# Performance work log

Hardware: AMD Instinct MI355X
Metric: run time of the kernel (lower is better)

Reference implementation:

```python
import jax, jax.numpy as jnp
import numpy as np

B, S, D = 32, 2048, 1024
E, K = 64, 8
N_TAGS = 128


def setup_inputs() -> dict:
    key = jax.random.key(0)
    k1, k2, k3, k4, k5, k6 = jax.random.split(key, 6)
    hidden_states = jax.random.normal(k1, (B, S, D), dtype=jnp.float32)
    subw_indices = jax.random.randint(k2, (B, E, K), 0, S, dtype=jnp.int32)
    subw_counts = jax.random.randint(k3, (B, E), 1, K + 1, dtype=jnp.int32)
    num_entities = jax.random.randint(k4, (B,), 1, E + 1, dtype=jnp.int32)
    fc_w = jax.random.normal(k5, (N_TAGS, D), dtype=jnp.float32) * (1.0 / np.sqrt(D))
    fc_b = jax.random.normal(k6, (N_TAGS,), dtype=jnp.float32) * 0.01
    return {
        "hidden_states": hidden_states,
        "subw_indices": subw_indices,
        "subw_counts": subw_counts,
        "num_entities": num_entities,
        "fc_w": fc_w,
        "fc_b": fc_b,
    }


def reference(hidden_states, subw_indices, subw_counts, num_entities, fc_w, fc_b):
    # Gather subword embeddings: [B, E, K, D]
    flat_idx = subw_indices.reshape(B, E * K)                      # [B, E*K]
    gathered = jnp.take_along_axis(
        hidden_states, flat_idx[:, :, None], axis=1
    ).reshape(B, E, K, D)
    # Mask padded subword slots and mean-pool per entity
    subw_mask = (jnp.arange(K)[None, None, :] < subw_counts[:, :, None])  # [B,E,K]
    subw_mask = subw_mask.astype(hidden_states.dtype)
    ent_emb = jnp.einsum("bekd,bek->bed", gathered, subw_mask)
    ent_emb = ent_emb / subw_counts[:, :, None].astype(hidden_states.dtype)
    # Zero-pad entities past num_entities (original pads with zero_emb)
    ent_mask = (jnp.arange(E)[None, :] < num_entities[:, None])    # [B,E]
    ent_emb = ent_emb * ent_mask[:, :, None].astype(hidden_states.dtype)
    # fc applied to all positions (padded rows yield the bias, as in original)
    logits = jnp.einsum("bed,td->bet", ent_emb, fc_w) + fc_b
    return logits
```

## Files before the change

### kernel.cpp

```cpp
#include <hip/hip_runtime.h>

#define BB 32
#define SS 2048
#define DD 1024
#define EE 64
#define KK 8
#define TT 128
#define MM (BB * EE)

#define KSPLIT 8
#define KCHUNK (DD / KSPLIT)
#define MT 32

typedef __attribute__((ext_vector_type(8))) short short8;
typedef __attribute__((ext_vector_type(4))) float f32x4;

__device__ __forceinline__ unsigned short f2bf(float f) {
    union { float f; unsigned int u; } v; v.f = f;
    unsigned int u = v.u + 0x7FFFu + ((v.u >> 16) & 1u);
    return (unsigned short)(u >> 16);
}

__global__ __launch_bounds__(256) void pool_kernel(
    const float* __restrict__ hs,
    const int*   __restrict__ subw_idx,
    const int*   __restrict__ subw_cnt,
    const int*   __restrict__ num_ent,
    const float* __restrict__ fc_w,
    unsigned short* __restrict__ entb,
    unsigned short* __restrict__ wb)
{
    const int be = blockIdx.x;
    const int b  = be >> 6;
    const int e  = be & 63;
    const int t  = threadIdx.x;

    const int cnt = subw_cnt[be];
    const int ne  = num_ent[b];
    const float scale = (e < ne) ? (1.0f / (float)cnt) : 0.0f;

    const int* idxp = subw_idx + (size_t)be * KK;

    float4 acc = make_float4(0.f, 0.f, 0.f, 0.f);
    #pragma unroll
    for (int k = 0; k < KK; ++k) {
        if (k < cnt) {
            const int s = idxp[k];
            const float4* row = (const float4*)(hs + ((size_t)b * SS + s) * DD);
            float4 v = row[t];
            acc.x += v.x; acc.y += v.y; acc.z += v.z; acc.w += v.w;
        }
    }
    ushort4 o;
    o.x = f2bf(acc.x * scale); o.y = f2bf(acc.y * scale);
    o.z = f2bf(acc.z * scale); o.w = f2bf(acc.w * scale);
    *(ushort4*)(entb + (size_t)be * DD + 4 * t) = o;

    if (t < 64) {
        const int j = be * 64 + t;
        wb[j] = f2bf(fc_w[j]);
    }
}

__global__ __launch_bounds__(256) void fc_mfma_kernel(
    const unsigned short* __restrict__ entb,
    const unsigned short* __restrict__ wb,
    float* __restrict__ part)
{
    __shared__ unsigned short As[MT][32];
    __shared__ unsigned short Bs[TT][32];

    const int bx = blockIdx.x;
    const int mt = bx >> 3;
    const int ks = bx & (KSPLIT - 1);
    const int t  = threadIdx.x;
    const int wid  = t >> 6;
    const int lane = t & 63;

    const int msub  = (wid & 1) * 16;
    const int nbase = (wid >> 1) * 64;

    const int k0 = ks * KCHUNK;

    f32x4 acc0 = {0.f,0.f,0.f,0.f}, acc1 = {0.f,0.f,0.f,0.f};
    f32x4 acc2 = {0.f,0.f,0.f,0.f}, acc3 = {0.f,0.f,0.f,0.f};

    const int lm = lane & 15;
    const int lq = (lane >> 4) * 8;

    for (int kc = 0; kc < KCHUNK; kc += 32) {
        if (t < 128) {
            const int m = t >> 2, s = t & 3;
            *(float4*)&As[m][s * 8] =
                *(const float4*)(entb + (size_t)(mt * MT + m) * DD + k0 + kc + s * 8);
        }
        #pragma unroll
        for (int j = 0; j < 2; ++j) {
            const int i = t + j * 256;
            const int n = i >> 2, s = i & 3;
            *(float4*)&Bs[n][s * 8] =
                *(const float4*)(wb + (size_t)n * DD + k0 + kc + s * 8);
        }
        __syncthreads();

        short8 a = *(const short8*)&As[msub + lm][lq];
        short8 b0 = *(const short8*)&Bs[nbase +  0 + lm][lq];
        short8 b1 = *(const short8*)&Bs[nbase + 16 + lm][lq];
        short8 b2 = *(const short8*)&Bs[nbase + 32 + lm][lq];
        short8 b3 = *(const short8*)&Bs[nbase + 48 + lm][lq];

        acc0 = __builtin_amdgcn_mfma_f32_16x16x32_bf16(a, b0, acc0, 0, 0, 0);
        acc1 = __builtin_amdgcn_mfma_f32_16x16x32_bf16(a, b1, acc1, 0, 0, 0);
        acc2 = __builtin_amdgcn_mfma_f32_16x16x32_bf16(a, b2, acc2, 0, 0, 0);
        acc3 = __builtin_amdgcn_mfma_f32_16x16x32_bf16(a, b3, acc3, 0, 0, 0);
        __syncthreads();
    }

    float* outp = part + (size_t)ks * MM * TT;
    const int mrow = mt * MT + msub + (lane >> 4) * 4;
    const int ncol = nbase + (lane & 15);
    #pragma unroll
    for (int r = 0; r < 4; ++r) {
        const size_t base = (size_t)(mrow + r) * TT + ncol;
        outp[base +  0] = acc0[r];
        outp[base + 16] = acc1[r];
        outp[base + 32] = acc2[r];
        outp[base + 48] = acc3[r];
    }
}

__global__ __launch_bounds__(256) void reduce_kernel(
    const float* __restrict__ part,
    const float* __restrict__ fc_b,
    float* __restrict__ out)
{
    const int i = blockIdx.x * 256 + threadIdx.x;
    float4 s = *(const float4*)(fc_b + (i & 31) * 4);
    #pragma unroll
    for (int k = 0; k < KSPLIT; ++k) {
        float4 p = *(const float4*)(part + (size_t)k * MM * TT + 4 * i);
        s.x += p.x; s.y += p.y; s.z += p.z; s.w += p.w;
    }
    *(float4*)(out + 4 * (size_t)i) = s;
}

extern "C" void kernel_launch(void* const* d_in, const int* in_sizes, int n_in,
                              void* d_out, int out_size, void* d_ws, size_t ws_size,
                              hipStream_t stream) {
    const float* hs       = (const float*)d_in[0];
    const int*   subw_idx = (const int*)  d_in[1];
    const int*   subw_cnt = (const int*)  d_in[2];
    const int*   num_ent  = (const int*)  d_in[3];
    const float* fc_w     = (const float*)d_in[4];
    const float* fc_b     = (const float*)d_in[5];
    float*       out      = (float*)d_out;

    unsigned short* entb = (unsigned short*)d_ws;
    unsigned short* wb   = (unsigned short*)((char*)d_ws + (size_t)MM * DD * 2);
    float*          part = (float*)((char*)d_ws + (size_t)MM * DD * 2 + (size_t)TT * DD * 2);

    pool_kernel<<<MM, 256, 0, stream>>>(hs, subw_idx, subw_cnt, num_ent,
                                        fc_w, entb, wb);
    fc_mfma_kernel<<<(MM / MT) * KSPLIT, 256, 0, stream>>>(entb, wb, part);
    reduce_kernel<<<(MM * TT / 4) / 256, 256, 0, stream>>>(part, fc_b, out);
}
```

Before: 318.4 us.

## Fuse entity pooling and weight conversion into the MFMA fc kernel

```diff
diff --git a/kernel.cpp b/kernel.cpp
--- a/kernel.cpp
+++ b/kernel.cpp
@@ -11,6 +11,7 @@
 #define KSPLIT 8
 #define KCHUNK (DD / KSPLIT)
 #define MT 32
+#define LSTR 136
 
 typedef __attribute__((ext_vector_type(8))) short short8;
 typedef __attribute__((ext_vector_type(4))) float f32x4;
@@ -21,54 +22,16 @@
     return (unsigned short)(u >> 16);
 }
 
-__global__ __launch_bounds__(256) void pool_kernel(
+__global__ __launch_bounds__(256) void fc_fused_kernel(
     const float* __restrict__ hs,
     const int*   __restrict__ subw_idx,
     const int*   __restrict__ subw_cnt,
     const int*   __restrict__ num_ent,
     const float* __restrict__ fc_w,
-    unsigned short* __restrict__ entb,
-    unsigned short* __restrict__ wb)
-{
-    const int be = blockIdx.x;
-    const int b  = be >> 6;
-    const int e  = be & 63;
-    const int t  = threadIdx.x;
-
-    const int cnt = subw_cnt[be];
-    const int ne  = num_ent[b];
-    const float scale = (e < ne) ? (1.0f / (float)cnt) : 0.0f;
-
-    const int* idxp = subw_idx + (size_t)be * KK;
-
-    float4 acc = make_float4(0.f, 0.f, 0.f, 0.f);
-    #pragma unroll
-    for (int k = 0; k < KK; ++k) {
-        if (k < cnt) {
-            const int s = idxp[k];
-            const float4* row = (const float4*)(hs + ((size_t)b * SS + s) * DD);
-            float4 v = row[t];
-            acc.x += v.x; acc.y += v.y; acc.z += v.z; acc.w += v.w;
-        }
-    }
-    ushort4 o;
-    o.x = f2bf(acc.x * scale); o.y = f2bf(acc.y * scale);
-    o.z = f2bf(acc.z * scale); o.w = f2bf(acc.w * scale);
-    *(ushort4*)(entb + (size_t)be * DD + 4 * t) = o;
-
-    if (t < 64) {
-        const int j = be * 64 + t;
-        wb[j] = f2bf(fc_w[j]);
-    }
-}
-
-__global__ __launch_bounds__(256) void fc_mfma_kernel(
-    const unsigned short* __restrict__ entb,
-    const unsigned short* __restrict__ wb,
     float* __restrict__ part)
 {
-    __shared__ unsigned short As[MT][32];
-    __shared__ unsigned short Bs[TT][32];
+    __shared__ unsigned short As[MT][LSTR];
+    __shared__ unsigned short Bs[TT][LSTR];
 
     const int bx = blockIdx.x;
     const int mt = bx >> 3;
@@ -76,44 +39,82 @@
     const int t  = threadIdx.x;
     const int wid  = t >> 6;
     const int lane = t & 63;
+    const int k0 = ks * KCHUNK;
+
+    {
+        const int r   = t >> 3;
+        const int sub = t & 7;
+        const int be  = mt * MT + r;
+        const int b   = be >> 6;
+        const int e   = be & 63;
+        const int cnt = subw_cnt[be];
+        const int ne  = num_ent[b];
+        const float scale = (e < ne) ? (1.0f / (float)cnt) : 0.0f;
+        const int* idxp = subw_idx + (size_t)be * KK;
+
+        float acc[16];
+        #pragma unroll
+        for (int j = 0; j < 16; ++j) acc[j] = 0.f;
+
+        for (int k = 0; k < cnt; ++k) {
+            const int s = idxp[k];
+            const float4* p = (const float4*)(hs + ((size_t)b * SS + s) * DD
+                                              + k0 + sub * 16);
+            #pragma unroll
+            for (int j = 0; j < 4; ++j) {
+                float4 v = p[j];
+                acc[4*j+0] += v.x; acc[4*j+1] += v.y;
+                acc[4*j+2] += v.z; acc[4*j+3] += v.w;
+            }
+        }
+        ushort4 o[4];
+        #pragma unroll
+        for (int j = 0; j < 4; ++j) {
+            o[j].x = f2bf(acc[4*j+0] * scale);
+            o[j].y = f2bf(acc[4*j+1] * scale);
+            o[j].z = f2bf(acc[4*j+2] * scale);
+            o[j].w = f2bf(acc[4*j+3] * scale);
+        }
+        *(ushort4*)&As[r][sub * 16 + 0]  = o[0];
+        *(ushort4*)&As[r][sub * 16 + 4]  = o[1];
+        *(ushort4*)&As[r][sub * 16 + 8]  = o[2];
+        *(ushort4*)&As[r][sub * 16 + 12] = o[3];
+    }
+
+    {
+        const int n = t >> 1;
+        const int h = (t & 1) * 64;
+        const float4* wrow = (const float4*)(fc_w + (size_t)n * DD + k0 + h);
+        #pragma unroll
+        for (int j = 0; j < 16; ++j) {
+            float4 v = wrow[j];
+            ushort4 o;
+            o.x = f2bf(v.x); o.y = f2bf(v.y); o.z = f2bf(v.z); o.w = f2bf(v.w);
+            *(ushort4*)&Bs[n][h + j * 4] = o;
+        }
+    }
+    __syncthreads();
 
     const int msub  = (wid & 1) * 16;
     const int nbase = (wid >> 1) * 64;
-
-    const int k0 = ks * KCHUNK;
+    const int lm = lane & 15;
+    const int lq = (lane >> 4) * 8;
 
     f32x4 acc0 = {0.f,0.f,0.f,0.f}, acc1 = {0.f,0.f,0.f,0.f};
     f32x4 acc2 = {0.f,0.f,0.f,0.f}, acc3 = {0.f,0.f,0.f,0.f};
 
-    const int lm = lane & 15;
-    const int lq = (lane >> 4) * 8;
-
-    for (int kc = 0; kc < KCHUNK; kc += 32) {
-        if (t < 128) {
-            const int m = t >> 2, s = t & 3;
-            *(float4*)&As[m][s * 8] =
-                *(const float4*)(entb + (size_t)(mt * MT + m) * DD + k0 + kc + s * 8);
-        }
-        #pragma unroll
-        for (int j = 0; j < 2; ++j) {
-            const int i = t + j * 256;
-            const int n = i >> 2, s = i & 3;
-            *(float4*)&Bs[n][s * 8] =
-                *(const float4*)(wb + (size_t)n * DD + k0 + kc + s * 8);
-        }
-        __syncthreads();
-
-        short8 a = *(const short8*)&As[msub + lm][lq];
-        short8 b0 = *(const short8*)&Bs[nbase +  0 + lm][lq];
-        short8 b1 = *(const short8*)&Bs[nbase + 16 + lm][lq];
-        short8 b2 = *(const short8*)&Bs[nbase + 32 + lm][lq];
-        short8 b3 = *(const short8*)&Bs[nbase + 48 + lm][lq];
-
+    #pragma unroll
+    for (int kstep = 0; kstep < KCHUNK / 32; ++kstep) {
+        const int kc = kstep * 32 + lq;
+        short8 a  = *(const short8*)&As[msub + lm][kc];
+        short8 b0 = *(const short8*)&Bs[nbase +  0 + lm][kc];
+        short8 b1 = *(const short8*)&Bs[nbase + 16 + lm][kc];
+        short8 b2 = *(const short8*)&Bs[nbase + 32 + lm][kc];
+        short8 b3 = *(const short8*)&Bs[nbase + 48 + lm][kc];
         acc0 = __builtin_amdgcn_mfma_f32_16x16x32_bf16(a, b0, acc0, 0, 0, 0);
         acc1 = __builtin_amdgcn_mfma_f32_16x16x32_bf16(a, b1, acc1, 0, 0, 0);
         acc2 = __builtin_amdgcn_mfma_f32_16x16x32_bf16(a, b2, acc2, 0, 0, 0);
         acc3 = __builtin_amdgcn_mfma_f32_16x16x32_bf16(a, b3, acc3, 0, 0, 0);
-        __syncthreads();
     }
 
     float* outp = part + (size_t)ks * MM * TT;
@@ -138,7 +139,7 @@
     float4 s = *(const float4*)(fc_b + (i & 31) * 4);
     #pragma unroll
     for (int k = 0; k < KSPLIT; ++k) {
-        float4 p = *(const float4*)(part + (size_t)k * MM * TT + 4 * i);
+        float4 p = *(const float4*)(part + (size_t)k * MM * TT + 4 * (size_t)i);
         s.x += p.x; s.y += p.y; s.z += p.z; s.w += p.w;
     }
     *(float4*)(out + 4 * (size_t)i) = s;
@@ -154,13 +155,9 @@
     const float* fc_w     = (const float*)d_in[4];
     const float* fc_b     = (const float*)d_in[5];
     float*       out      = (float*)d_out;
+    float*       part     = (float*)d_ws;
 
-    unsigned short* entb = (unsigned short*)d_ws;
-    unsigned short* wb   = (unsigned short*)((char*)d_ws + (size_t)MM * DD * 2);
-    float*          part = (float*)((char*)d_ws + (size_t)MM * DD * 2 + (size_t)TT * DD * 2);
-
-    pool_kernel<<<MM, 256, 0, stream>>>(hs, subw_idx, subw_cnt, num_ent,
-                                        fc_w, entb, wb);
-    fc_mfma_kernel<<<(MM / MT) * KSPLIT, 256, 0, stream>>>(entb, wb, part);
+    fc_fused_kernel<<<(MM / MT) * KSPLIT, 256, 0, stream>>>(
+        hs, subw_idx, subw_cnt, num_ent, fc_w, part);
     reduce_kernel<<<(MM * TT / 4) / 256, 256, 0, stream>>>(part, fc_b, out);
 }
```

New measurement: 318.2 us. Within noise of the previous version (-0.1%).
